# Performance work log

Measured on AMD Instinct MI355X. Metric: run time of the kernel, lower is better.

The kernel has to match this reference:

```python
import jax, jax.numpy as jnp
import numpy as np
import math

B, T, E, H, R = 4, 1024, 1024, 16, 16
DH = E // H


def setup_inputs() -> dict:
    key = jax.random.key(0)
    ks = jax.random.split(key, 14)
    s = 0.02
    inp = {
        "X": jax.random.normal(ks[0], (B, T, E), dtype=jnp.float32),
        "mask": jnp.ones((B, T), dtype=jnp.float32),
        # full-rank frozen projections (torch Linear: y = x @ W.T + b)
        "Wq": jax.random.normal(ks[1], (E, E), dtype=jnp.float32) * s,
        "bq": jnp.zeros((E,), dtype=jnp.float32),
        "Wk": jax.random.normal(ks[2], (E, E), dtype=jnp.float32) * s,
        "bk": jnp.zeros((E,), dtype=jnp.float32),
        "Wv": jax.random.normal(ks[3], (E, E), dtype=jnp.float32) * s,
        "bv": jnp.zeros((E,), dtype=jnp.float32),
        # LoRA: A: [R, E], B: [E, R], no bias
        "Aq": jax.random.normal(ks[4], (R, E), dtype=jnp.float32) * s,
        "Bq": jax.random.normal(ks[5], (E, R), dtype=jnp.float32) * s,
        "Ak": jax.random.normal(ks[6], (R, E), dtype=jnp.float32) * s,
        "Bk": jax.random.normal(ks[7], (E, R), dtype=jnp.float32) * s,
        "Av": jax.random.normal(ks[8], (R, E), dtype=jnp.float32) * s,
        "Bv": jax.random.normal(ks[9], (E, R), dtype=jnp.float32) * s,
    }
    return inp


def _split_heads(x):
    # [B, T, E] -> [B, H, T, Dh]
    b, t, _ = x.shape
    return x.reshape(b, t, H, DH).transpose(0, 2, 1, 3)


def reference(X, mask, Wq, bq, Wk, bk, Wv, bv, Aq, Bq, Ak, Bk, Av, Bv):
    def proj(W, b, A, Bl):
        # frozen linear + LoRA: X @ W.T + b + (X @ A.T) @ B.T
        return X @ W.T + b + (X @ A.T) @ Bl.T

    q = _split_heads(proj(Wq, bq, Aq, Bq))  # [B,H,T,Dh]
    k = _split_heads(proj(Wk, bk, Ak, Bk))
    v = _split_heads(proj(Wv, bv, Av, Bv))

    t = q.shape[2]
    scores = jnp.einsum("bhid,bhjd->bhij", q, k) / math.sqrt(E)
    # causal: positions with col > row set to -inf (triu offset=1)
    causal = jnp.triu(jnp.ones((t, t), dtype=bool), k=1)
    scores = jnp.where(causal, -jnp.inf, scores)
    # NOTE: faithful to source: softmax over axis=dims-2 (query/row axis)
    attn = jax.nn.softmax(scores, axis=2)
    # post-softmax padding-mask multiply, broadcast [B,1,1,T]
    attn = attn * mask[:, None, None, :]
    out = jnp.einsum("bhij,bhjd->bhid", attn, v)  # [B,H,T,Dh]
    return out.transpose(0, 2, 1, 3).reshape(X.shape[0], t, E)
```

## Files before the change

kernel.cpp:

```cpp
#include <hip/hip_runtime.h>
#include <stdint.h>

typedef __bf16 v8bf __attribute__((ext_vector_type(8)));
typedef float  v4f  __attribute__((ext_vector_type(4)));

__device__ __forceinline__ uint16_t f2bf(float f){
  union { float f; uint32_t u; } v; v.f = f;
  uint32_t r = v.u + 0x7FFFu + ((v.u >> 16) & 1u);
  return (uint16_t)(r >> 16);
}
__device__ __forceinline__ float bf2f(uint16_t u){
  union { uint32_t u; float f; } v; v.u = ((uint32_t)u) << 16; return v.f;
}
__device__ __forceinline__ v4f vzero(){ v4f z = {0.f,0.f,0.f,0.f}; return z; }

__device__ __forceinline__ void gld16(const uint16_t* __restrict__ g, uint16_t* l){
  __builtin_amdgcn_global_load_lds((const __attribute__((address_space(1))) void*)g,
                                   (__attribute__((address_space(3))) void*)l, 16, 0, 0);
}

__device__ __forceinline__ void ld64(uint4 r[2], const uint16_t* __restrict__ g, int ldg, int tid){
  int row = tid >> 2, c = (tid & 3) * 16;
  r[0] = *(const uint4*)(g + (size_t)row * ldg + c);
  r[1] = *(const uint4*)(g + (size_t)row * ldg + c + 8);
}
__device__ __forceinline__ void st64(uint16_t* __restrict__ s, const uint4 r[2], int tid){
  int row = tid >> 2, c = (tid & 3) * 16;
  *(uint4*)(s + row * 72 + c) = r[0];
  *(uint4*)(s + row * 72 + c + 8) = r[1];
}
__device__ __forceinline__ void stage64(uint16_t* s, const uint16_t* g, int ldg, int tid){
  uint4 r[2]; ld64(r, g, ldg, tid); st64(s, r, tid);
}

__global__ void k_xcast(const float* __restrict__ X, uint16_t* __restrict__ Xb,
                        float* __restrict__ csum){
  int i = (blockIdx.x * 256 + threadIdx.x) * 8;
  float4 a = *(const float4*)(X + i);
  float4 b = *(const float4*)(X + i + 4);
  union { uint16_t h[8]; uint4 v; } o;
  o.h[0]=f2bf(a.x); o.h[1]=f2bf(a.y); o.h[2]=f2bf(a.z); o.h[3]=f2bf(a.w);
  o.h[4]=f2bf(b.x); o.h[5]=f2bf(b.y); o.h[6]=f2bf(b.z); o.h[7]=f2bf(b.w);
  *(uint4*)(Xb + i) = o.v;
  if (blockIdx.x < 64)
    ((float4*)csum)[blockIdx.x * 256 + threadIdx.x] = make_float4(0.f, 0.f, 0.f, 0.f);
}

__global__ void k_weff(const float* __restrict__ Wq, const float* __restrict__ Aq, const float* __restrict__ Bq,
                       const float* __restrict__ Wk, const float* __restrict__ Ak, const float* __restrict__ Bk,
                       const float* __restrict__ Wv, const float* __restrict__ Av, const float* __restrict__ Bv,
                       uint16_t* __restrict__ Wo){
  int y = blockIdx.y;
  const float* W  = (y == 0) ? Wq : (y == 1) ? Wk : Wv;
  const float* A  = (y == 0) ? Aq : (y == 1) ? Ak : Av;
  const float* Bm = (y == 0) ? Bq : (y == 1) ? Bk : Bv;
  int idx = blockIdx.x * 256 + threadIdx.x;
  int f = idx >> 10, k = idx & 1023;
  float acc = W[idx];
  #pragma unroll
  for (int r = 0; r < 16; ++r) acc += Bm[f * 16 + r] * A[r * 1024 + k];
  Wo[(size_t)y * 1048576 + idx] = f2bf(acc);
}

__global__ __launch_bounds__(256, 4)
void k_gemm(const uint16_t* __restrict__ Ag, const uint16_t* __restrict__ Bg,
            const float* __restrict__ qb, const float* __restrict__ kb,
            const float* __restrict__ vb, uint16_t* __restrict__ Cg){
  __shared__ __align__(16) uint16_t smem[16896];
  uint16_t* As = smem;
  uint16_t* Bs = smem + 8192;
  int tid = threadIdx.x, lane = tid & 63, wid = tid >> 6;
  int l15 = lane & 15, lg = lane >> 4;
  int wr = wid >> 1, wc = wid & 1;
  int bid = blockIdx.x, xcd = bid & 7, idx = bid >> 3;
  int nb = xcd * 96 + idx;
  int mt = nb / 24, nt = nb - mt * 24;
  int m0 = mt * 128, n0 = nt * 128;

  int lr  = lane >> 3;
  int lcs = (((lane & 7) ^ lr)) * 8;
  const uint16_t* Abase = Ag + (size_t)(m0 + wid * 32 + lr) * 1024 + lcs;
  const uint16_t* Bbase = Bg + (size_t)(n0 + wid * 32 + lr) * 1024 + lcs;
  uint16_t* Alds = As + wid * 32 * 64;
  uint16_t* Blds = Bs + wid * 32 * 64;

  int sw = l15 & 7;

  v4f acc[4][4];
  #pragma unroll
  for (int a = 0; a < 4; ++a)
    #pragma unroll
    for (int c = 0; c < 4; ++c) acc[a][c] = vzero();

  for (int kk = 0; kk < 1024; kk += 64){
    __syncthreads();
    #pragma unroll
    for (int i = 0; i < 4; ++i){
      gld16(Abase + (size_t)(i * 8) * 1024 + kk, Alds + i * 8 * 64);
      gld16(Bbase + (size_t)(i * 8) * 1024 + kk, Blds + i * 8 * 64);
    }
    __syncthreads();
    #pragma unroll
    for (int kc = 0; kc < 2; ++kc){
      v8bf af[4], bfr[4];
      int cs = ((kc * 4 + lg) ^ sw) * 8;
      #pragma unroll
      for (int mi = 0; mi < 4; ++mi)
        af[mi] = *(const v8bf*)(As + (wr * 64 + mi * 16 + l15) * 64 + cs);
      #pragma unroll
      for (int nj = 0; nj < 4; ++nj)
        bfr[nj] = *(const v8bf*)(Bs + (wc * 64 + nj * 16 + l15) * 64 + cs);
      #pragma unroll
      for (int mi = 0; mi < 4; ++mi)
        #pragma unroll
        for (int nj = 0; nj < 4; ++nj)
          acc[mi][nj] = __builtin_amdgcn_mfma_f32_16x16x32_bf16(af[mi], bfr[nj], acc[mi][nj], 0, 0, 0);
    }
  }
  __syncthreads();
  uint16_t* Ct = smem;
  #pragma unroll
  for (int nj = 0; nj < 4; ++nj){
    int n = n0 + wc * 64 + nj * 16 + l15;
    float bv_ = (n < 1024) ? qb[n] : (n < 2048) ? kb[n - 1024] : vb[n - 2048];
    #pragma unroll
    for (int mi = 0; mi < 4; ++mi)
      #pragma unroll
      for (int r = 0; r < 4; ++r){
        int ml = wr * 64 + mi * 16 + lg * 4 + r;
        Ct[ml * 132 + wc * 64 + nj * 16 + l15] = f2bf(acc[mi][nj][r] + bv_);
      }
  }
  __syncthreads();
  {
    int row = tid >> 1;
    int c0  = (tid & 1) * 64;
    uint16_t* gp = Cg + (size_t)(m0 + row) * 3072 + n0 + c0;
    const uint16_t* sp = Ct + row * 132 + c0;
    #pragma unroll
    for (int c = 0; c < 8; ++c)
      *(uint4*)(gp + c * 8) = *(const uint4*)(sp + c * 8);
  }
}

__global__ __launch_bounds__(256, 4)
void k_score(const uint16_t* __restrict__ QKVg, float* __restrict__ csum,
             uint16_t* __restrict__ Pws){
  __shared__ __align__(16) uint16_t Ka[4096], Kb2[4096], Qs[4096];
  int tid = threadIdx.x, lane = tid & 63, wid = tid >> 6;
  int l15 = lane & 15, lg = lane >> 4;
  int wr = wid >> 1, wc = wid & 1;
  int sw = l15 & 7;
  int bid = blockIdx.x, xcd = bid & 7, idx = bid >> 3;
  int bh = xcd * 8 + (idx & 7);
  int rest = idx >> 3;
  int pr = rest & 7, ph = rest >> 3;
  int b = bh >> 4, h = bh & 15;
  int jtA = pr, jtB = 15 - pr;
  const uint16_t* Qb = QKVg + (size_t)b * 1024 * 3072 + h * 64;
  const uint16_t* Kb = QKVg + (size_t)b * 1024 * 3072 + 1024 + h * 64;
  uint16_t* Pbh = Pws + (size_t)bh * 557056;

  int lr  = lane >> 3;
  int lcs = ((lane & 7) ^ lr) * 8;
  {
    const uint16_t* sA = Kb + (size_t)(jtA * 64 + wid * 16 + lr) * 3072 + lcs;
    const uint16_t* sB = Kb + (size_t)(jtB * 64 + wid * 16 + lr) * 3072 + lcs;
    gld16(sA, Ka + wid * 16 * 64);
    gld16(sA + (size_t)8 * 3072, Ka + (wid * 16 + 8) * 64);
    gld16(sB, Kb2 + wid * 16 * 64);
    gld16(sB + (size_t)8 * 3072, Kb2 + (wid * 16 + 8) * 64);
  }
  int it0 = jtA + ph;
  v4f cpA[2] = {vzero(), vzero()}, cpB[2] = {vzero(), vzero()};
  for (int it = it0; it < 16; it += 2){
    __syncthreads();
    {
      const uint16_t* sQ = Qb + (size_t)(it * 64 + wid * 16 + lr) * 3072 + lcs;
      gld16(sQ, Qs + wid * 16 * 64);
      gld16(sQ + (size_t)8 * 3072, Qs + (wid * 16 + 8) * 64);
    }
    __syncthreads();
    bool doB = (it >= jtB);
    v4f sa[2][2], sb[2][2];
    #pragma unroll
    for (int a = 0; a < 2; ++a)
      #pragma unroll
      for (int c = 0; c < 2; ++c){ sa[a][c] = vzero(); sb[a][c] = vzero(); }
    #pragma unroll
    for (int kc = 0; kc < 2; ++kc){
      int cs = ((kc * 4 + lg) ^ sw) * 8;
      v8bf aq[2], k1[2], k2[2];
      #pragma unroll
      for (int ni = 0; ni < 2; ++ni)
        aq[ni] = *(const v8bf*)(Qs + (wc * 32 + ni * 16 + l15) * 64 + cs);
      #pragma unroll
      for (int mj = 0; mj < 2; ++mj)
        k1[mj] = *(const v8bf*)(Ka + (wr * 32 + mj * 16 + l15) * 64 + cs);
      __builtin_amdgcn_s_setprio(1);
      #pragma unroll
      for (int mj = 0; mj < 2; ++mj)
        #pragma unroll
        for (int ni = 0; ni < 2; ++ni)
          sa[mj][ni] = __builtin_amdgcn_mfma_f32_16x16x32_bf16(k1[mj], aq[ni], sa[mj][ni], 0, 0, 0);
      __builtin_amdgcn_s_setprio(0);
      if (doB){
        #pragma unroll
        for (int mj = 0; mj < 2; ++mj)
          k2[mj] = *(const v8bf*)(Kb2 + (wr * 32 + mj * 16 + l15) * 64 + cs);
        __builtin_amdgcn_s_setprio(1);
        #pragma unroll
        for (int mj = 0; mj < 2; ++mj)
          #pragma unroll
          for (int ni = 0; ni < 2; ++ni)
            sb[mj][ni] = __builtin_amdgcn_mfma_f32_16x16x32_bf16(k2[mj], aq[ni], sb[mj][ni], 0, 0, 0);
        __builtin_amdgcn_s_setprio(0);
      }
    }
    bool diagA = (it == jtA), diagB = (it == jtB);
    int tri = it * (it + 1) / 2;
    uint16_t* dA = Pbh + (size_t)(tri + jtA) * 4096;
    uint16_t* dB = Pbh + (size_t)(tri + jtB) * 4096;
    #pragma unroll
    for (int mj = 0; mj < 2; ++mj)
      #pragma unroll
      for (int ni = 0; ni < 2; ++ni){
        int iL = wc * 32 + ni * 16 + l15;
        int jb = wr * 32 + mj * 16 + lg * 4;
        int off = iL * 64 + (((jb >> 3) ^ (iL & 7)) * 8) + (jb & 7);
        {
          float e0 = (!diagA || jb + 0 <= iL) ? __expf(sa[mj][ni][0] * 0.03125f) : 0.f;
          float e1 = (!diagA || jb + 1 <= iL) ? __expf(sa[mj][ni][1] * 0.03125f) : 0.f;
          float e2 = (!diagA || jb + 2 <= iL) ? __expf(sa[mj][ni][2] * 0.03125f) : 0.f;
          float e3 = (!diagA || jb + 3 <= iL) ? __expf(sa[mj][ni][3] * 0.03125f) : 0.f;
          v4f e4 = {e0, e1, e2, e3};
          cpA[mj] += e4;
          uint2 pk;
          pk.x = (uint32_t)f2bf(e0) | ((uint32_t)f2bf(e1) << 16);
          pk.y = (uint32_t)f2bf(e2) | ((uint32_t)f2bf(e3) << 16);
          *(uint2*)(dA + off) = pk;
        }
        if (doB){
          float e0 = (!diagB || jb + 0 <= iL) ? __expf(sb[mj][ni][0] * 0.03125f) : 0.f;
          float e1 = (!diagB || jb + 1 <= iL) ? __expf(sb[mj][ni][1] * 0.03125f) : 0.f;
          float e2 = (!diagB || jb + 2 <= iL) ? __expf(sb[mj][ni][2] * 0.03125f) : 0.f;
          float e3 = (!diagB || jb + 3 <= iL) ? __expf(sb[mj][ni][3] * 0.03125f) : 0.f;
          v4f e4 = {e0, e1, e2, e3};
          cpB[mj] += e4;
          uint2 pk;
          pk.x = (uint32_t)f2bf(e0) | ((uint32_t)f2bf(e1) << 16);
          pk.y = (uint32_t)f2bf(e2) | ((uint32_t)f2bf(e3) << 16);
          *(uint2*)(dB + off) = pk;
        }
      }
  }
  #pragma unroll
  for (int mj = 0; mj < 2; ++mj)
    #pragma unroll
    for (int m = 1; m <= 8; m <<= 1)
      #pragma unroll
      for (int r = 0; r < 4; ++r){
        cpA[mj][r] += __shfl_xor(cpA[mj][r], m, 64);
        cpB[mj][r] += __shfl_xor(cpB[mj][r], m, 64);
      }
  if (l15 == 0){
    #pragma unroll
    for (int mj = 0; mj < 2; ++mj)
      #pragma unroll
      for (int r = 0; r < 4; ++r){
        int jo = wr * 32 + mj * 16 + lg * 4 + r;
        atomicAdd(&csum[(size_t)bh * 1024 + jtA * 64 + jo], cpA[mj][r]);
        atomicAdd(&csum[(size_t)bh * 1024 + jtB * 64 + jo], cpB[mj][r]);
      }
  }
}

__global__ __launch_bounds__(256)
void k_vprep(const uint16_t* __restrict__ QKVg, const float* __restrict__ csum,
             const float* __restrict__ mask, uint16_t* __restrict__ Vp){
  __shared__ __align__(16) uint16_t Vs[128 * 72];
  __shared__ float scb[128];
  int tid = threadIdx.x;
  int bid = blockIdx.x, xcd = bid & 7, idx = bid >> 3;
  int bh = xcd * 8 + (idx & 7);
  int jt = idx >> 3;
  int b = bh >> 4, h = bh & 15;
  int j0 = jt * 128;
  stage64(Vs,           QKVg + ((size_t)(b * 1024 + j0)) * 3072 + 2048 + h * 64, 3072, tid);
  stage64(Vs + 64 * 72, QKVg + ((size_t)(b * 1024 + j0 + 64)) * 3072 + 2048 + h * 64, 3072, tid);
  if (tid < 128) scb[tid] = mask[b * 1024 + j0 + tid] / csum[(size_t)bh * 1024 + j0 + tid];
  __syncthreads();
  int d = tid >> 2, jc = (tid & 3) * 32;
  #pragma unroll
  for (int g8 = 0; g8 < 4; ++g8){
    union { uint16_t h[8]; uint4 v; } o;
    #pragma unroll
    for (int e = 0; e < 8; ++e){
      int j = jc + g8 * 8 + e;
      o.h[e] = f2bf(bf2f(Vs[j * 72 + d]) * scb[j]);
    }
    int jl = jc + g8 * 8;
    int wbase = jl & ~63;
    int c = (jl & 63) >> 3;
    int jphys = wbase + ((c ^ (d & 7)) * 8);
    *(uint4*)(Vp + (size_t)bh * 65536 + (size_t)d * 1024 + j0 + jphys) = o.v;
  }
}

__global__ __launch_bounds__(256, 4)
void k_pv(const uint16_t* __restrict__ Pws, const uint16_t* __restrict__ Vp,
          float* __restrict__ out){
  __shared__ __align__(16) float Of[64 * 68];
  int tid = threadIdx.x, lane = tid & 63, l15 = lane & 15, lg = lane >> 4, wid = tid >> 6;
  int sw = l15 & 7;
  int bid = blockIdx.x, xcd = bid & 7, idx = bid >> 3;
  int bh = xcd * 8 + (idx & 7);
  int it = idx >> 3;
  int b = bh >> 4, h = bh & 15;
  const uint16_t* Pbh = Pws + (size_t)bh * 557056 + (size_t)(it * (it + 1) / 2) * 4096
                      + (wid * 16 + l15) * 64;
  const uint16_t* Vb  = Vp + (size_t)bh * 65536;
  v4f oacc[4];
  #pragma unroll
  for (int c = 0; c < 4; ++c) oacc[c] = vzero();

  #pragma unroll 2
  for (int jt = 0; jt <= it; ++jt){
    const uint16_t* pt = Pbh + (size_t)jt * 4096;
    const uint16_t* vt = Vb + jt * 64;
    #pragma unroll
    for (int kc = 0; kc < 2; ++kc){
      int cs = ((kc * 4 + lg) ^ sw) * 8;
      v8bf pa = *(const v8bf*)(pt + cs);
      v8bf vb_[4];
      #pragma unroll
      for (int dj = 0; dj < 4; ++dj)
        vb_[dj] = *(const v8bf*)(vt + (size_t)(dj * 16 + l15) * 1024 + cs);
      __builtin_amdgcn_s_setprio(1);
      #pragma unroll
      for (int dj = 0; dj < 4; ++dj)
        oacc[dj] = __builtin_amdgcn_mfma_f32_16x16x32_bf16(pa, vb_[dj], oacc[dj], 0, 0, 0);
      __builtin_amdgcn_s_setprio(0);
    }
  }
  #pragma unroll
  for (int dj = 0; dj < 4; ++dj)
    #pragma unroll
    for (int r = 0; r < 4; ++r)
      Of[(wid * 16 + lg * 4 + r) * 68 + dj * 16 + l15] = oacc[dj][r];
  __syncthreads();
  {
    int row = tid >> 2, c0 = (tid & 3) * 16;
    float* gp = out + ((size_t)(b * 1024) + it * 64 + row) * 1024 + h * 64 + c0;
    const float* sp = Of + row * 68 + c0;
    #pragma unroll
    for (int c = 0; c < 4; ++c)
      *(float4*)(gp + c * 4) = *(const float4*)(sp + c * 4);
  }
}

extern "C" void kernel_launch(void* const* d_in, const int* in_sizes, int n_in,
                              void* d_out, int out_size, void* d_ws, size_t ws_size,
                              hipStream_t stream) {
  (void)in_sizes; (void)n_in; (void)out_size; (void)ws_size;
  const float* X    = (const float*)d_in[0];
  const float* mask = (const float*)d_in[1];
  const float* Wq   = (const float*)d_in[2];
  const float* bq   = (const float*)d_in[3];
  const float* Wk   = (const float*)d_in[4];
  const float* bk   = (const float*)d_in[5];
  const float* Wv   = (const float*)d_in[6];
  const float* bv   = (const float*)d_in[7];
  const float* Aq   = (const float*)d_in[8];
  const float* Bq   = (const float*)d_in[9];
  const float* Ak   = (const float*)d_in[10];
  const float* Bk   = (const float*)d_in[11];
  const float* Av   = (const float*)d_in[12];
  const float* Bv   = (const float*)d_in[13];
  float* out = (float*)d_out;

  uint16_t* Xb   = (uint16_t*)d_ws;
  uint16_t* Weff = Xb + (size_t)4096 * 1024;
  uint16_t* QKV  = Weff + (size_t)3 * 1024 * 1024;
  uint16_t* Vp   = QKV + (size_t)4096 * 3072;
  float*    csum = (float*)(Vp + (size_t)64 * 64 * 1024);
  uint16_t* Pws  = (uint16_t*)((char*)d_ws + 48496640ULL);

  k_xcast<<<2048, 256, 0, stream>>>(X, Xb, csum);
  k_weff<<<dim3(4096, 3), 256, 0, stream>>>(Wq, Aq, Bq, Wk, Ak, Bk, Wv, Av, Bv, Weff);
  k_gemm<<<768, 256, 0, stream>>>(Xb, Weff, bq, bk, bv, QKV);
  k_score<<<1024, 256, 0, stream>>>(QKV, csum, Pws);
  k_vprep<<<512, 256, 0, stream>>>(QKV, csum, mask, Vp);
  k_pv<<<1024, 256, 0, stream>>>(Pws, Vp, out);
}
```

Before: 111.5 us.

## Merge prep kernels, stage score tiles via LDS, double-buffer PV loads

Merges the X cast and the LoRA weight-merge kernels into one launch, removing a kernel boundary. The score kernel now writes its exp tiles into LDS first and then copies them to global memory with coalesced 16-byte stores instead of scattered 8-byte stores, at the cost of an extra barrier and more LDS. The PV kernel now double-buffers its P and V tiles in LDS using async global-to-LDS loads rather than reading strided global memory directly. The larger LDS footprint may reduce occupancy.

Measured after the change: 100.9 us. 9.5% less time.

```diff
diff --git a/kernel.cpp b/kernel.cpp
--- a/kernel.cpp
+++ b/kernel.cpp
@@ -33,33 +33,36 @@
   uint4 r[2]; ld64(r, g, ldg, tid); st64(s, r, tid);
 }
 
-__global__ void k_xcast(const float* __restrict__ X, uint16_t* __restrict__ Xb,
-                        float* __restrict__ csum){
-  int i = (blockIdx.x * 256 + threadIdx.x) * 8;
-  float4 a = *(const float4*)(X + i);
-  float4 b = *(const float4*)(X + i + 4);
-  union { uint16_t h[8]; uint4 v; } o;
-  o.h[0]=f2bf(a.x); o.h[1]=f2bf(a.y); o.h[2]=f2bf(a.z); o.h[3]=f2bf(a.w);
-  o.h[4]=f2bf(b.x); o.h[5]=f2bf(b.y); o.h[6]=f2bf(b.z); o.h[7]=f2bf(b.w);
-  *(uint4*)(Xb + i) = o.v;
-  if (blockIdx.x < 64)
-    ((float4*)csum)[blockIdx.x * 256 + threadIdx.x] = make_float4(0.f, 0.f, 0.f, 0.f);
-}
-
-__global__ void k_weff(const float* __restrict__ Wq, const float* __restrict__ Aq, const float* __restrict__ Bq,
+__global__ void k_prep(const float* __restrict__ X, uint16_t* __restrict__ Xb,
+                       float* __restrict__ csum,
+                       const float* __restrict__ Wq, const float* __restrict__ Aq, const float* __restrict__ Bq,
                        const float* __restrict__ Wk, const float* __restrict__ Ak, const float* __restrict__ Bk,
                        const float* __restrict__ Wv, const float* __restrict__ Av, const float* __restrict__ Bv,
                        uint16_t* __restrict__ Wo){
-  int y = blockIdx.y;
-  const float* W  = (y == 0) ? Wq : (y == 1) ? Wk : Wv;
-  const float* A  = (y == 0) ? Aq : (y == 1) ? Ak : Av;
-  const float* Bm = (y == 0) ? Bq : (y == 1) ? Bk : Bv;
-  int idx = blockIdx.x * 256 + threadIdx.x;
-  int f = idx >> 10, k = idx & 1023;
-  float acc = W[idx];
-  #pragma unroll
-  for (int r = 0; r < 16; ++r) acc += Bm[f * 16 + r] * A[r * 1024 + k];
-  Wo[(size_t)y * 1048576 + idx] = f2bf(acc);
+  int bid = blockIdx.x, tid = threadIdx.x;
+  if (bid < 2048){
+    int i = (bid * 256 + tid) * 8;
+    float4 a = *(const float4*)(X + i);
+    float4 b = *(const float4*)(X + i + 4);
+    union { uint16_t h[8]; uint4 v; } o;
+    o.h[0]=f2bf(a.x); o.h[1]=f2bf(a.y); o.h[2]=f2bf(a.z); o.h[3]=f2bf(a.w);
+    o.h[4]=f2bf(b.x); o.h[5]=f2bf(b.y); o.h[6]=f2bf(b.z); o.h[7]=f2bf(b.w);
+    *(uint4*)(Xb + i) = o.v;
+    if (bid < 64)
+      ((float4*)csum)[bid * 256 + tid] = make_float4(0.f, 0.f, 0.f, 0.f);
+  } else {
+    int w = bid - 2048;
+    int y = w >> 12;
+    const float* W  = (y == 0) ? Wq : (y == 1) ? Wk : Wv;
+    const float* A  = (y == 0) ? Aq : (y == 1) ? Ak : Av;
+    const float* Bm = (y == 0) ? Bq : (y == 1) ? Bk : Bv;
+    int idx = (w & 4095) * 256 + tid;
+    int f = idx >> 10, k = idx & 1023;
+    float acc = W[idx];
+    #pragma unroll
+    for (int r = 0; r < 16; ++r) acc += Bm[f * 16 + r] * A[r * 1024 + k];
+    Wo[(size_t)y * 1048576 + idx] = f2bf(acc);
+  }
 }
 
 __global__ __launch_bounds__(256, 4)
@@ -146,7 +149,7 @@
 __global__ __launch_bounds__(256, 4)
 void k_score(const uint16_t* __restrict__ QKVg, float* __restrict__ csum,
              uint16_t* __restrict__ Pws){
-  __shared__ __align__(16) uint16_t Ka[4096], Kb2[4096], Qs[4096];
+  __shared__ __align__(16) uint16_t Ka[4096], Kb2[4096], Qs[4096], PsA[4096], PsB[4096];
   int tid = threadIdx.x, lane = tid & 63, wid = tid >> 6;
   int l15 = lane & 15, lg = lane >> 4;
   int wr = wid >> 1, wc = wid & 1;
@@ -218,9 +221,6 @@
       }
     }
     bool diagA = (it == jtA), diagB = (it == jtB);
-    int tri = it * (it + 1) / 2;
-    uint16_t* dA = Pbh + (size_t)(tri + jtA) * 4096;
-    uint16_t* dB = Pbh + (size_t)(tri + jtB) * 4096;
     #pragma unroll
     for (int mj = 0; mj < 2; ++mj)
       #pragma unroll
@@ -238,7 +238,7 @@
           uint2 pk;
           pk.x = (uint32_t)f2bf(e0) | ((uint32_t)f2bf(e1) << 16);
           pk.y = (uint32_t)f2bf(e2) | ((uint32_t)f2bf(e3) << 16);
-          *(uint2*)(dA + off) = pk;
+          *(uint2*)(PsA + off) = pk;
         }
         if (doB){
           float e0 = (!diagB || jb + 0 <= iL) ? __expf(sb[mj][ni][0] * 0.03125f) : 0.f;
@@ -250,9 +250,23 @@
           uint2 pk;
           pk.x = (uint32_t)f2bf(e0) | ((uint32_t)f2bf(e1) << 16);
           pk.y = (uint32_t)f2bf(e2) | ((uint32_t)f2bf(e3) << 16);
-          *(uint2*)(dB + off) = pk;
+          *(uint2*)(PsB + off) = pk;
         }
       }
+    __syncthreads();
+    {
+      int tri = it * (it + 1) / 2;
+      uint16_t* dA = Pbh + (size_t)(tri + jtA) * 4096 + tid * 16;
+      uint4 a0 = *(const uint4*)(PsA + tid * 16);
+      uint4 a1 = *(const uint4*)(PsA + tid * 16 + 8);
+      *(uint4*)dA = a0; *(uint4*)(dA + 8) = a1;
+      if (doB){
+        uint16_t* dB = Pbh + (size_t)(tri + jtB) * 4096 + tid * 16;
+        uint4 b0 = *(const uint4*)(PsB + tid * 16);
+        uint4 b1 = *(const uint4*)(PsB + tid * 16 + 8);
+        *(uint4*)dB = b0; *(uint4*)(dB + 8) = b1;
+      }
+    }
   }
   #pragma unroll
   for (int mj = 0; mj < 2; ++mj)
@@ -310,39 +324,56 @@
 __global__ __launch_bounds__(256, 4)
 void k_pv(const uint16_t* __restrict__ Pws, const uint16_t* __restrict__ Vp,
           float* __restrict__ out){
-  __shared__ __align__(16) float Of[64 * 68];
+  __shared__ __align__(16) uint16_t smem[16384];
   int tid = threadIdx.x, lane = tid & 63, l15 = lane & 15, lg = lane >> 4, wid = tid >> 6;
   int sw = l15 & 7;
   int bid = blockIdx.x, xcd = bid & 7, idx = bid >> 3;
   int bh = xcd * 8 + (idx & 7);
   int it = idx >> 3;
   int b = bh >> 4, h = bh & 15;
-  const uint16_t* Pbh = Pws + (size_t)bh * 557056 + (size_t)(it * (it + 1) / 2) * 4096
-                      + (wid * 16 + l15) * 64;
+  const uint16_t* Pbh = Pws + (size_t)bh * 557056 + (size_t)(it * (it + 1) / 2) * 4096;
   const uint16_t* Vb  = Vp + (size_t)bh * 65536;
   v4f oacc[4];
   #pragma unroll
   for (int c = 0; c < 4; ++c) oacc[c] = vzero();
 
-  #pragma unroll 2
+  #define PV_STAGE(buf, jt) do {                                                        \
+    uint16_t* Pt_ = smem + (buf) * 8192;                                                \
+    uint16_t* Vt_ = Pt_ + 4096;                                                         \
+    const uint16_t* ps = Pbh + (size_t)(jt) * 4096;                                     \
+    gld16(ps + wid * 512 + lane * 8,        Pt_ + wid * 512);                           \
+    gld16(ps + 2048 + wid * 512 + lane * 8, Pt_ + 2048 + wid * 512);                    \
+    const uint16_t* vs = Vb + (size_t)(jt) * 64;                                        \
+    gld16(vs + (size_t)(wid * 8 + (lane >> 3)) * 1024 + (lane & 7) * 8,      Vt_ + wid * 512); \
+    gld16(vs + (size_t)(32 + wid * 8 + (lane >> 3)) * 1024 + (lane & 7) * 8, Vt_ + 2048 + wid * 512); \
+  } while (0)
+
+  PV_STAGE(0, 0);
+  __syncthreads();
+  int cur = 0;
   for (int jt = 0; jt <= it; ++jt){
-    const uint16_t* pt = Pbh + (size_t)jt * 4096;
-    const uint16_t* vt = Vb + jt * 64;
+    if (jt < it) PV_STAGE(cur ^ 1, jt + 1);
+    const uint16_t* Pt = smem + cur * 8192;
+    const uint16_t* Vt = Pt + 4096;
     #pragma unroll
     for (int kc = 0; kc < 2; ++kc){
       int cs = ((kc * 4 + lg) ^ sw) * 8;
-      v8bf pa = *(const v8bf*)(pt + cs);
+      v8bf pa = *(const v8bf*)(Pt + (wid * 16 + l15) * 64 + cs);
       v8bf vb_[4];
       #pragma unroll
       for (int dj = 0; dj < 4; ++dj)
-        vb_[dj] = *(const v8bf*)(vt + (size_t)(dj * 16 + l15) * 1024 + cs);
+        vb_[dj] = *(const v8bf*)(Vt + (dj * 16 + l15) * 64 + cs);
       __builtin_amdgcn_s_setprio(1);
       #pragma unroll
       for (int dj = 0; dj < 4; ++dj)
         oacc[dj] = __builtin_amdgcn_mfma_f32_16x16x32_bf16(pa, vb_[dj], oacc[dj], 0, 0, 0);
       __builtin_amdgcn_s_setprio(0);
     }
-  }
+    __syncthreads();
+    cur ^= 1;
+  }
+  #undef PV_STAGE
+  float* Of = (float*)smem;
   #pragma unroll
   for (int dj = 0; dj < 4; ++dj)
     #pragma unroll
@@ -386,8 +417,7 @@
   float*    csum = (float*)(Vp + (size_t)64 * 64 * 1024);
   uint16_t* Pws  = (uint16_t*)((char*)d_ws + 48496640ULL);
 
-  k_xcast<<<2048, 256, 0, stream>>>(X, Xb, csum);
-  k_weff<<<dim3(4096, 3), 256, 0, stream>>>(Wq, Aq, Bq, Wk, Ak, Bk, Wv, Av, Bv, Weff);
+  k_prep<<<14336, 256, 0, stream>>>(X, Xb, csum, Wq, Aq, Bq, Wk, Ak, Bk, Wv, Av, Bv, Weff);
   k_gemm<<<768, 256, 0, stream>>>(Xb, Weff, bq, bk, bv, QKV);
   k_score<<<1024, 256, 0, stream>>>(QKV, csum, Pws);
   k_vprep<<<512, 256, 0, stream>>>(QKV, csum, mask, Vp);
```
